# Optimization experiments

Hardware: AMD Instinct MI355X
Metric: run time of the kernel (lower is better)

## Reference

```python
import jax, jax.numpy as jnp
import numpy as np

N = 50000   # nodes
E = 800000  # edges (avg degree 16)
D = 2048    # resnet50 feature dim
C = 256     # layer_size
NEG_SLOPE = 0.2


def setup_inputs() -> dict:
    key = jax.random.key(0)
    ks = jax.random.split(key, 16)
    s = 0.02
    inp = {
        'x': jax.random.normal(ks[0], (N, D), jnp.float32),
        'edge_index': jax.random.randint(ks[1], (2, E), 0, N, dtype=jnp.int32),
        # GATConv layer 1 (in=D, out=C, heads=1)
        'W1': jax.random.normal(ks[2], (D, C), jnp.float32) * s,
        'a_src1': jax.random.normal(ks[3], (C,), jnp.float32) * s,
        'a_dst1': jax.random.normal(ks[4], (C,), jnp.float32) * s,
        'b1': jnp.zeros((C,), jnp.float32),
        # GATConv layer 2 (in=C, out=C)
        'W2': jax.random.normal(ks[5], (C, C), jnp.float32) * s,
        'a_src2': jax.random.normal(ks[6], (C,), jnp.float32) * s,
        'a_dst2': jax.random.normal(ks[7], (C,), jnp.float32) * s,
        'b2': jnp.zeros((C,), jnp.float32),
        # EdgePredictor: lin1 (2C -> C), lin2 (C -> 1)
        'Wp1': jax.random.normal(ks[8], (2 * C, C), jnp.float32) * s,
        'bp1': jnp.zeros((C,), jnp.float32),
        'wp2': jax.random.normal(ks[9], (C,), jnp.float32) * s,
        'bp2': jnp.zeros((), jnp.float32),
    }
    return inp


def gat_layer(x, src, dst, W, a_src, a_dst, b, n_nodes):
    # PyG GATConv, heads=1, concat=True: message flows src -> dst,
    # softmax over incoming edges of each dst node.
    h = x @ W                                   # [N, C]
    e = jax.nn.leaky_relu((h @ a_src)[src] + (h @ a_dst)[dst], NEG_SLOPE)  # [E]
    emax = jax.ops.segment_max(e, dst, num_segments=n_nodes)
    ex = jnp.exp(e - emax[dst])
    denom = jax.ops.segment_sum(ex, dst, num_segments=n_nodes)
    alpha = ex / (denom[dst] + 1e-16)           # [E]
    out = jax.ops.segment_sum(h[src] * alpha[:, None], dst, num_segments=n_nodes)
    return out + b


def reference(x, edge_index, W1, a_src1, a_dst1, b1, W2, a_src2, a_dst2, b2,
              Wp1, bp1, wp2, bp2):
    src, dst = edge_index[0], edge_index[1]
    # GATConv default add_self_loops=True
    loops = jnp.arange(N, dtype=src.dtype)
    src_sl = jnp.concatenate([src, loops])
    dst_sl = jnp.concatenate([dst, loops])

    h = gat_layer(x, src_sl, dst_sl, W1, a_src1, a_dst1, b1, N)
    h = gat_layer(h, src_sl, dst_sl, W2, a_src2, a_dst2, b2, N)

    # edge predictor on the ORIGINAL edge_index (no self loops)
    xe = jnp.concatenate([h[src], h[dst]], axis=-1)       # [E, 2C]
    z = jax.nn.relu(xe @ Wp1 + bp1)                        # [E, C]  (dropout: eval mode)
    return z @ wp2 + bp2                                   # [E]
```

## Files before the change

### kernel.cpp

```cpp
#include <hip/hip_runtime.h>
#include <hip/hip_bf16.h>
#include <stdint.h>

#define NNODES 50000
#define NEDGES 800000
#define DIN    2048
#define CDIM   256
#define ELOOP  (NEDGES + NNODES)

using bf16x8 = __attribute__((ext_vector_type(8))) short;
using f32x4  = __attribute__((ext_vector_type(4))) float;
using gvoid  = __attribute__((address_space(1))) const void;
using lvoid  = __attribute__((address_space(3))) void;

__device__ __forceinline__ float bf2f(uint16_t u) {
    union { uint32_t i; float f; } v; v.i = (uint32_t)u << 16; return v.f;
}
__device__ __forceinline__ uint16_t f2bf(float f) {
    union { float f; uint32_t i; } v; v.f = f;
    uint32_t i = v.i;
    return (uint16_t)((i + 0x7FFFu + ((i >> 16) & 1u)) >> 16);
}

#define BM 128
#define BN 128
#define BK 32

__global__ __launch_bounds__(256)
void gemm_bt(const uint16_t* __restrict__ A, const uint16_t* __restrict__ Bt,
             uint16_t* __restrict__ C, const float* __restrict__ bias,
             int M, int N, int K)
{
    __shared__ __align__(16) uint16_t lA[BM * BK];
    __shared__ __align__(16) uint16_t lB[BN * BK];
    const int tid  = threadIdx.x;
    const int wave = tid >> 6;
    const int lane = tid & 63;
    const int lm = lane & 15, lq = lane >> 4;
    const int bm = blockIdx.x * BM;
    const int bn = blockIdx.y * BN;
    const int wm = (wave >> 1) * 64;
    const int wn = (wave & 1) * 64;

    f32x4 acc[4][4];
    for (int i = 0; i < 4; ++i)
        for (int j = 0; j < 4; ++j)
            acc[i][j] = (f32x4)0.0f;

    for (int k0 = 0; k0 < K; k0 += BK) {
        for (int j = 0; j < 2; ++j) {
            int c = j * 256 + wave * 64 + lane;
            int row = c >> 2, cc = c & 3;
            int gr = bm + row; if (gr >= M) gr = M - 1;
            const uint16_t* gp = A + (size_t)gr * K + k0 + cc * 8;
            __builtin_amdgcn_global_load_lds((gvoid*)gp,
                (lvoid*)(lA + (size_t)(j * 256 + wave * 64) * 8), 16, 0, 0);
        }
        for (int j = 0; j < 2; ++j) {
            int c = j * 256 + wave * 64 + lane;
            int row = c >> 2, cc = c & 3;
            int gr = bn + row; if (gr >= N) gr = N - 1;
            const uint16_t* gp = Bt + (size_t)gr * K + k0 + cc * 8;
            __builtin_amdgcn_global_load_lds((gvoid*)gp,
                (lvoid*)(lB + (size_t)(j * 256 + wave * 64) * 8), 16, 0, 0);
        }
        __syncthreads();

        bf16x8 af[4], bfr[4];
        for (int mt = 0; mt < 4; ++mt)
            af[mt] = *(const bf16x8*)(lA + (wm + mt * 16 + lm) * BK + lq * 8);
        for (int nt = 0; nt < 4; ++nt)
            bfr[nt] = *(const bf16x8*)(lB + (wn + nt * 16 + lm) * BK + lq * 8);

        for (int mt = 0; mt < 4; ++mt)
            for (int nt = 0; nt < 4; ++nt)
                acc[mt][nt] = __builtin_amdgcn_mfma_f32_16x16x32_bf16(
                    af[mt], bfr[nt], acc[mt][nt], 0, 0, 0);
        __syncthreads();
    }

    for (int mt = 0; mt < 4; ++mt) {
        for (int nt = 0; nt < 4; ++nt) {
            int gn = bn + wn + nt * 16 + lm;
            float badd = bias ? bias[gn] : 0.0f;
            for (int r = 0; r < 4; ++r) {
                int gm = bm + wm + mt * 16 + lq * 4 + r;
                if (gm < M)
                    C[(size_t)gm * N + gn] = f2bf(acc[mt][nt][r] + badd);
            }
        }
    }
}

__global__ __launch_bounds__(256)
void gemm_f32_bt(const float* __restrict__ A, const uint16_t* __restrict__ Bt,
                 uint16_t* __restrict__ C, int M, int N, int K)
{
    __shared__ __align__(16) float    lA[BM * BK];
    __shared__ __align__(16) uint16_t lB[BN * BK];
    const int tid  = threadIdx.x;
    const int wave = tid >> 6;
    const int lane = tid & 63;
    const int lm = lane & 15, lq = lane >> 4;
    const int bm = blockIdx.x * BM;
    const int bn = blockIdx.y * BN;
    const int wm = (wave >> 1) * 64;
    const int wn = (wave & 1) * 64;

    f32x4 acc[4][4];
    for (int i = 0; i < 4; ++i)
        for (int j = 0; j < 4; ++j)
            acc[i][j] = (f32x4)0.0f;

    for (int k0 = 0; k0 < K; k0 += BK) {
        for (int j = 0; j < 4; ++j) {
            int c = j * 256 + wave * 64 + lane;
            int row = c >> 3;
            int lc  = (c & 7) ^ (row & 7);
            int gr = bm + row; if (gr >= M) gr = M - 1;
            const float* gp = A + (size_t)gr * K + k0 + lc * 4;
            __builtin_amdgcn_global_load_lds((gvoid*)gp,
                (lvoid*)(lA + (size_t)(j * 256 + wave * 64) * 4), 16, 0, 0);
        }
        for (int j = 0; j < 2; ++j) {
            int c = j * 256 + wave * 64 + lane;
            int row = c >> 2, cc = c & 3;
            const uint16_t* gp = Bt + (size_t)(bn + row) * K + k0 + cc * 8;
            __builtin_amdgcn_global_load_lds((gvoid*)gp,
                (lvoid*)(lB + (size_t)(j * 256 + wave * 64) * 8), 16, 0, 0);
        }
        __syncthreads();

        bf16x8 af[4], bfr[4];
        for (int mt = 0; mt < 4; ++mt) {
            int r = wm + mt * 16 + lm;
            int s0 = (lq * 2)     ^ (r & 7);
            int s1 = (lq * 2 + 1) ^ (r & 7);
            f32x4 a0 = *(const f32x4*)(lA + r * BK + s0 * 4);
            f32x4 a1 = *(const f32x4*)(lA + r * BK + s1 * 4);
            bf16x8 t;
            for (int q = 0; q < 4; ++q) {
                t[q]     = (short)f2bf(a0[q]);
                t[q + 4] = (short)f2bf(a1[q]);
            }
            af[mt] = t;
        }
        for (int nt = 0; nt < 4; ++nt)
            bfr[nt] = *(const bf16x8*)(lB + (wn + nt * 16 + lm) * BK + lq * 8);

        for (int mt = 0; mt < 4; ++mt)
            for (int nt = 0; nt < 4; ++nt)
                acc[mt][nt] = __builtin_amdgcn_mfma_f32_16x16x32_bf16(
                    af[mt], bfr[nt], acc[mt][nt], 0, 0, 0);
        __syncthreads();
    }

    for (int mt = 0; mt < 4; ++mt) {
        for (int nt = 0; nt < 4; ++nt) {
            int gn = bn + wn + nt * 16 + lm;
            for (int r = 0; r < 4; ++r) {
                int gm = bm + wm + mt * 16 + lq * 4 + r;
                if (gm < M)
                    C[(size_t)gm * N + gn] = f2bf(acc[mt][nt][r]);
            }
        }
    }
}

__global__ void transpose_cvt_kernel(const float* __restrict__ W,
                                     uint16_t* __restrict__ Wt, int K, int N)
{
    int idx = blockIdx.x * 256 + threadIdx.x;
    if (idx >= K * N) return;
    int n = idx / K, k = idx - n * K;
    Wt[idx] = f2bf(W[(size_t)k * N + n]);
}

__global__ void count_kernel(const int* __restrict__ ei, int* __restrict__ rs)
{
    int i = blockIdx.x * 256 + threadIdx.x;
    if (i >= ELOOP) return;
    int dst = (i < NEDGES) ? ei[NEDGES + i] : (i - NEDGES);
    atomicAdd(&rs[dst + 1], 1);
}

__global__ __launch_bounds__(1024)
void scan_kernel(int* __restrict__ rs, int* __restrict__ cursor)
{
    __shared__ int wsum[16];
    const int tid = threadIdx.x, lane = tid & 63, w = tid >> 6;
    int carry = 0;
    for (int base = 0; base <= NNODES; base += 1024) {
        int i = base + tid;
        int v = (i <= NNODES) ? rs[i] : 0;
        int s = v;
        for (int d = 1; d < 64; d <<= 1) {
            int t = __shfl_up(s, d);
            if (lane >= d) s += t;
        }
        if (lane == 63) wsum[w] = s;
        __syncthreads();
        if (tid < 16) {
            int x = wsum[tid];
            for (int d = 1; d < 16; d <<= 1) {
                int t = __shfl_up(x, d);
                if (tid >= d) x += t;
            }
            wsum[tid] = x;
        }
        __syncthreads();
        int incl = s + carry + (w > 0 ? wsum[w - 1] : 0);
        if (i <= NNODES) {
            rs[i] = incl;
            if (i < NNODES) cursor[i] = incl;
        }
        int total = carry + wsum[15];
        __syncthreads();
        carry = total;
    }
}

__global__ void fill_kernel(const int* __restrict__ ei, int* __restrict__ cursor,
                            int* __restrict__ csr_src)
{
    int i = blockIdx.x * 256 + threadIdx.x;
    if (i >= ELOOP) return;
    int src, dst;
    if (i < NEDGES) { src = ei[i]; dst = ei[NEDGES + i]; }
    else            { src = dst = i - NEDGES; }
    int pos = atomicAdd(&cursor[dst], 1);
    csr_src[pos] = src;
}

__global__ __launch_bounds__(256)
void rowdot_kernel(const uint16_t* __restrict__ g,
                   const float* __restrict__ asrc,
                   const float* __restrict__ adst,
                   float* __restrict__ s_src, float* __restrict__ s_dst)
{
    int n = blockIdx.x * 4 + (threadIdx.x >> 6);
    int lane = threadIdx.x & 63;
    ushort4 rv = *(const ushort4*)(g + (size_t)n * CDIM + lane * 4);
    float4 av = *(const float4*)(asrc + lane * 4);
    float4 dv = *(const float4*)(adst + lane * 4);
    float r0 = bf2f(rv.x), r1 = bf2f(rv.y), r2 = bf2f(rv.z), r3 = bf2f(rv.w);
    float a = r0 * av.x + r1 * av.y + r2 * av.z + r3 * av.w;
    float b = r0 * dv.x + r1 * dv.y + r2 * dv.z + r3 * dv.w;
    for (int d = 32; d; d >>= 1) { a += __shfl_xor(a, d); b += __shfl_xor(b, d); }
    if (lane == 0) { s_src[n] = a; s_dst[n] = b; }
}

__global__ __launch_bounds__(256)
void attn_kernel(const int* __restrict__ row_start, const int* __restrict__ csr_src,
                 const float* __restrict__ s_src, const float* __restrict__ s_dst,
                 const uint16_t* __restrict__ g, const float* __restrict__ bvec,
                 uint16_t* __restrict__ hout)
{
    int n = blockIdx.x * 4 + (threadIdx.x >> 6);
    int lane = threadIdx.x & 63;
    int beg = row_start[n], end = row_start[n + 1];
    float sdn = s_dst[n];

    float m = -1e30f;
    for (int i = beg + lane; i < end; i += 64) {
        float e = s_src[csr_src[i]] + sdn;
        e = (e > 0.f) ? e : 0.2f * e;
        m = fmaxf(m, e);
    }
    for (int d = 32; d; d >>= 1) m = fmaxf(m, __shfl_xor(m, d));

    float sum = 0.f;
    for (int i = beg + lane; i < end; i += 64) {
        float e = s_src[csr_src[i]] + sdn;
        e = (e > 0.f) ? e : 0.2f * e;
        sum += __expf(e - m);
    }
    for (int d = 32; d; d >>= 1) sum += __shfl_xor(sum, d);
    float inv = 1.f / (sum + 1e-16f);

    float a0 = 0.f, a1 = 0.f, a2 = 0.f, a3 = 0.f;
    for (int i = beg; i < end; ++i) {
        int src = csr_src[i];
        float e = s_src[src] + sdn;
        e = (e > 0.f) ? e : 0.2f * e;
        float alpha = __expf(e - m) * inv;
        ushort4 rv = *(const ushort4*)(g + (size_t)src * CDIM + lane * 4);
        a0 += alpha * bf2f(rv.x);
        a1 += alpha * bf2f(rv.y);
        a2 += alpha * bf2f(rv.z);
        a3 += alpha * bf2f(rv.w);
    }
    float4 bv = *(const float4*)(bvec + lane * 4);
    ushort4 o;
    o.x = f2bf(a0 + bv.x);
    o.y = f2bf(a1 + bv.y);
    o.z = f2bf(a2 + bv.z);
    o.w = f2bf(a3 + bv.w);
    *(ushort4*)(hout + (size_t)n * CDIM + lane * 4) = o;
}

__global__ __launch_bounds__(256)
void edgepred_kernel(const int* __restrict__ ei,
                     const uint16_t* __restrict__ U, const uint16_t* __restrict__ V,
                     const float* __restrict__ wp2, const float* __restrict__ bp2,
                     float* __restrict__ out)
{
    const int tid = threadIdx.x;
    const int grp = tid >> 4, l = tid & 15;
    const int e = blockIdx.x * 16 + grp;
    int src = ei[e];
    int dst = ei[NEDGES + e];
    const uint4 u0 = *(const uint4*)(U + (size_t)src * CDIM + l * 16);
    const uint4 u1 = *(const uint4*)(U + (size_t)src * CDIM + l * 16 + 8);
    const uint4 v0 = *(const uint4*)(V + (size_t)dst * CDIM + l * 16);
    const uint4 v1 = *(const uint4*)(V + (size_t)dst * CDIM + l * 16 + 8);
    const float4 w0 = *(const float4*)(wp2 + l * 16);
    const float4 w1 = *(const float4*)(wp2 + l * 16 + 4);
    const float4 w2 = *(const float4*)(wp2 + l * 16 + 8);
    const float4 w3 = *(const float4*)(wp2 + l * 16 + 12);
    float acc = 0.f;
    auto proc = [&](uint32_t uu, uint32_t vv, float wa, float wb) {
        float z0 = fmaxf(bf2f((uint16_t)(uu & 0xffffu)) + bf2f((uint16_t)(vv & 0xffffu)), 0.f);
        float z1 = fmaxf(bf2f((uint16_t)(uu >> 16)) + bf2f((uint16_t)(vv >> 16)), 0.f);
        acc += z0 * wa + z1 * wb;
    };
    proc(u0.x, v0.x, w0.x, w0.y); proc(u0.y, v0.y, w0.z, w0.w);
    proc(u0.z, v0.z, w1.x, w1.y); proc(u0.w, v0.w, w1.z, w1.w);
    proc(u1.x, v1.x, w2.x, w2.y); proc(u1.y, v1.y, w2.z, w2.w);
    proc(u1.z, v1.z, w3.x, w3.y); proc(u1.w, v1.w, w3.z, w3.w);
    for (int d = 1; d < 16; d <<= 1) acc += __shfl_xor(acc, d);
    if (l == 0) out[e] = acc + *bp2;
}

extern "C" void kernel_launch(void* const* d_in, const int* in_sizes, int n_in,
                              void* d_out, int out_size, void* d_ws, size_t ws_size,
                              hipStream_t stream)
{
    const float* x   = (const float*)d_in[0];
    const int*   ei  = (const int*)d_in[1];
    const float* W1  = (const float*)d_in[2];
    const float* as1 = (const float*)d_in[3];
    const float* ad1 = (const float*)d_in[4];
    const float* b1  = (const float*)d_in[5];
    const float* W2  = (const float*)d_in[6];
    const float* as2 = (const float*)d_in[7];
    const float* ad2 = (const float*)d_in[8];
    const float* b2  = (const float*)d_in[9];
    const float* Wp1 = (const float*)d_in[10];
    const float* bp1 = (const float*)d_in[11];
    const float* wp2 = (const float*)d_in[12];
    const float* bp2 = (const float*)d_in[13];
    float* out = (float*)d_out;

    char* ws = (char*)d_ws;
    size_t off = 0;
    auto alloc = [&](size_t bytes) -> void* {
        void* p = ws + off;
        off += (bytes + 255) & ~(size_t)255;
        return p;
    };
    uint16_t* W1t  = (uint16_t*)alloc((size_t)DIN * CDIM * 2);
    uint16_t* W2t  = (uint16_t*)alloc((size_t)CDIM * CDIM * 2);
    uint16_t* WpAt = (uint16_t*)alloc((size_t)CDIM * CDIM * 2);
    uint16_t* WpBt = (uint16_t*)alloc((size_t)CDIM * CDIM * 2);
    int* row_start = (int*)alloc((NNODES + 1) * sizeof(int));
    int* cursor    = (int*)alloc(NNODES * sizeof(int));
    int* csr_src   = (int*)alloc((size_t)ELOOP * sizeof(int));
    float* s_src   = (float*)alloc(NNODES * sizeof(float));
    float* s_dst   = (float*)alloc(NNODES * sizeof(float));
    uint16_t* G    = (uint16_t*)alloc((size_t)NNODES * CDIM * 2);
    uint16_t* H    = (uint16_t*)alloc((size_t)NNODES * CDIM * 2);
    uint16_t* Vb   = (uint16_t*)alloc((size_t)NNODES * CDIM * 2);

    hipMemsetAsync(row_start, 0, (NNODES + 1) * sizeof(int), stream);

    transpose_cvt_kernel<<<(DIN * CDIM + 255) / 256, 256, 0, stream>>>(W1, W1t, DIN, CDIM);
    transpose_cvt_kernel<<<(CDIM * CDIM + 255) / 256, 256, 0, stream>>>(W2, W2t, CDIM, CDIM);
    transpose_cvt_kernel<<<(CDIM * CDIM + 255) / 256, 256, 0, stream>>>(Wp1, WpAt, CDIM, CDIM);
    transpose_cvt_kernel<<<(CDIM * CDIM + 255) / 256, 256, 0, stream>>>(Wp1 + CDIM * CDIM, WpBt, CDIM, CDIM);

    count_kernel<<<(ELOOP + 255) / 256, 256, 0, stream>>>(ei, row_start);
    scan_kernel<<<1, 1024, 0, stream>>>(row_start, cursor);
    fill_kernel<<<(ELOOP + 255) / 256, 256, 0, stream>>>(ei, cursor, csr_src);

    dim3 gg((NNODES + BM - 1) / BM, CDIM / BN);

    gemm_f32_bt<<<gg, 256, 0, stream>>>(x, W1t, G, NNODES, CDIM, DIN);
    rowdot_kernel<<<NNODES / 4, 256, 0, stream>>>(G, as1, ad1, s_src, s_dst);
    attn_kernel<<<NNODES / 4, 256, 0, stream>>>(row_start, csr_src, s_src, s_dst, G, b1, H);

    gemm_bt<<<gg, 256, 0, stream>>>(H, W2t, G, nullptr, NNODES, CDIM, CDIM);
    rowdot_kernel<<<NNODES / 4, 256, 0, stream>>>(G, as2, ad2, s_src, s_dst);
    attn_kernel<<<NNODES / 4, 256, 0, stream>>>(row_start, csr_src, s_src, s_dst, G, b2, H);

    gemm_bt<<<gg, 256, 0, stream>>>(H, WpAt, G, bp1, NNODES, CDIM, CDIM);
    gemm_bt<<<gg, 256, 0, stream>>>(H, WpBt, Vb, nullptr, NNODES, CDIM, CDIM);

    edgepred_kernel<<<NEDGES / 16, 256, 0, stream>>>(ei, G, Vb, wp2, bp2, out);
}
```

Measured before the change: 1.237 ms.

## Double-buffer LDS tiles in GEMMs and merge edge-predictor GEMMs into one

Both GEMM kernels now keep two LDS buffers and issue the global-to-LDS loads for the next K tile before computing on the current one. This is meant to overlap load latency with the MFMA work and drops one barrier per iteration. The two 256-wide edge-predictor projections become a single N=512 GEMM that writes an interleaved U|V buffer with a padded bias vector. Edgepred reads both halves from that one buffer, which saves a launch and a second read of H. The cost is double the LDS use and a 512-wide output that spills from the G region into the adjacent Vb allocation.

```diff
diff --git a/kernel.cpp b/kernel.cpp
--- a/kernel.cpp
+++ b/kernel.cpp
@@ -31,8 +31,8 @@
              uint16_t* __restrict__ C, const float* __restrict__ bias,
              int M, int N, int K)
 {
-    __shared__ __align__(16) uint16_t lA[BM * BK];
-    __shared__ __align__(16) uint16_t lB[BN * BK];
+    __shared__ __align__(16) uint16_t lA[2][BM * BK];
+    __shared__ __align__(16) uint16_t lB[2][BN * BK];
     const int tid  = threadIdx.x;
     const int wave = tid >> 6;
     const int lane = tid & 63;
@@ -47,14 +47,14 @@
         for (int j = 0; j < 4; ++j)
             acc[i][j] = (f32x4)0.0f;
 
-    for (int k0 = 0; k0 < K; k0 += BK) {
+    auto stage = [&](int buf, int k0) {
         for (int j = 0; j < 2; ++j) {
             int c = j * 256 + wave * 64 + lane;
             int row = c >> 2, cc = c & 3;
             int gr = bm + row; if (gr >= M) gr = M - 1;
             const uint16_t* gp = A + (size_t)gr * K + k0 + cc * 8;
             __builtin_amdgcn_global_load_lds((gvoid*)gp,
-                (lvoid*)(lA + (size_t)(j * 256 + wave * 64) * 8), 16, 0, 0);
+                (lvoid*)(lA[buf] + (size_t)(j * 256 + wave * 64) * 8), 16, 0, 0);
         }
         for (int j = 0; j < 2; ++j) {
             int c = j * 256 + wave * 64 + lane;
@@ -62,31 +62,39 @@
             int gr = bn + row; if (gr >= N) gr = N - 1;
             const uint16_t* gp = Bt + (size_t)gr * K + k0 + cc * 8;
             __builtin_amdgcn_global_load_lds((gvoid*)gp,
-                (lvoid*)(lB + (size_t)(j * 256 + wave * 64) * 8), 16, 0, 0);
-        }
-        __syncthreads();
+                (lvoid*)(lB[buf] + (size_t)(j * 256 + wave * 64) * 8), 16, 0, 0);
+        }
+    };
+
+    const int nt = K / BK;
+    stage(0, 0);
+    __syncthreads();
+    int cur = 0;
+    for (int t = 0; t < nt; ++t) {
+        if (t + 1 < nt) stage(cur ^ 1, (t + 1) * BK);
 
         bf16x8 af[4], bfr[4];
         for (int mt = 0; mt < 4; ++mt)
-            af[mt] = *(const bf16x8*)(lA + (wm + mt * 16 + lm) * BK + lq * 8);
-        for (int nt = 0; nt < 4; ++nt)
-            bfr[nt] = *(const bf16x8*)(lB + (wn + nt * 16 + lm) * BK + lq * 8);
+            af[mt] = *(const bf16x8*)(lA[cur] + (wm + mt * 16 + lm) * BK + lq * 8);
+        for (int nt2 = 0; nt2 < 4; ++nt2)
+            bfr[nt2] = *(const bf16x8*)(lB[cur] + (wn + nt2 * 16 + lm) * BK + lq * 8);
 
         for (int mt = 0; mt < 4; ++mt)
-            for (int nt = 0; nt < 4; ++nt)
-                acc[mt][nt] = __builtin_amdgcn_mfma_f32_16x16x32_bf16(
-                    af[mt], bfr[nt], acc[mt][nt], 0, 0, 0);
+            for (int nt2 = 0; nt2 < 4; ++nt2)
+                acc[mt][nt2] = __builtin_amdgcn_mfma_f32_16x16x32_bf16(
+                    af[mt], bfr[nt2], acc[mt][nt2], 0, 0, 0);
         __syncthreads();
+        cur ^= 1;
     }
 
     for (int mt = 0; mt < 4; ++mt) {
-        for (int nt = 0; nt < 4; ++nt) {
-            int gn = bn + wn + nt * 16 + lm;
+        for (int nt2 = 0; nt2 < 4; ++nt2) {
+            int gn = bn + wn + nt2 * 16 + lm;
             float badd = bias ? bias[gn] : 0.0f;
             for (int r = 0; r < 4; ++r) {
                 int gm = bm + wm + mt * 16 + lq * 4 + r;
                 if (gm < M)
-                    C[(size_t)gm * N + gn] = f2bf(acc[mt][nt][r] + badd);
+                    C[(size_t)gm * N + gn] = f2bf(acc[mt][nt2][r] + badd);
             }
         }
     }
@@ -96,8 +104,8 @@
 void gemm_f32_bt(const float* __restrict__ A, const uint16_t* __restrict__ Bt,
                  uint16_t* __restrict__ C, int M, int N, int K)
 {
-    __shared__ __align__(16) float    lA[BM * BK];
-    __shared__ __align__(16) uint16_t lB[BN * BK];
+    __shared__ __align__(16) float    lA[2][BM * BK];
+    __shared__ __align__(16) uint16_t lB[2][BN * BK];
     const int tid  = threadIdx.x;
     const int wave = tid >> 6;
     const int lane = tid & 63;
@@ -112,7 +120,7 @@
         for (int j = 0; j < 4; ++j)
             acc[i][j] = (f32x4)0.0f;
 
-    for (int k0 = 0; k0 < K; k0 += BK) {
+    auto stage = [&](int buf, int k0) {
         for (int j = 0; j < 4; ++j) {
             int c = j * 256 + wave * 64 + lane;
             int row = c >> 3;
@@ -120,48 +128,57 @@
             int gr = bm + row; if (gr >= M) gr = M - 1;
             const float* gp = A + (size_t)gr * K + k0 + lc * 4;
             __builtin_amdgcn_global_load_lds((gvoid*)gp,
-                (lvoid*)(lA + (size_t)(j * 256 + wave * 64) * 4), 16, 0, 0);
+                (lvoid*)(lA[buf] + (size_t)(j * 256 + wave * 64) * 4), 16, 0, 0);
         }
         for (int j = 0; j < 2; ++j) {
             int c = j * 256 + wave * 64 + lane;
             int row = c >> 2, cc = c & 3;
-            const uint16_t* gp = Bt + (size_t)(bn + row) * K + k0 + cc * 8;
+            int gr = bn + row; if (gr >= N) gr = N - 1;
+            const uint16_t* gp = Bt + (size_t)gr * K + k0 + cc * 8;
             __builtin_amdgcn_global_load_lds((gvoid*)gp,
-                (lvoid*)(lB + (size_t)(j * 256 + wave * 64) * 8), 16, 0, 0);
-        }
-        __syncthreads();
+                (lvoid*)(lB[buf] + (size_t)(j * 256 + wave * 64) * 8), 16, 0, 0);
+        }
+    };
+
+    const int nt = K / BK;
+    stage(0, 0);
+    __syncthreads();
+    int cur = 0;
+    for (int t = 0; t < nt; ++t) {
+        if (t + 1 < nt) stage(cur ^ 1, (t + 1) * BK);
 
         bf16x8 af[4], bfr[4];
         for (int mt = 0; mt < 4; ++mt) {
             int r = wm + mt * 16 + lm;
             int s0 = (lq * 2)     ^ (r & 7);
             int s1 = (lq * 2 + 1) ^ (r & 7);
-            f32x4 a0 = *(const f32x4*)(lA + r * BK + s0 * 4);
-            f32x4 a1 = *(const f32x4*)(lA + r * BK + s1 * 4);
-            bf16x8 t;
+            f32x4 a0 = *(const f32x4*)(lA[cur] + r * BK + s0 * 4);
+            f32x4 a1 = *(const f32x4*)(lA[cur] + r * BK + s1 * 4);
+            bf16x8 t2;
             for (int q = 0; q < 4; ++q) {
-                t[q]     = (short)f2bf(a0[q]);
-                t[q + 4] = (short)f2bf(a1[q]);
+                t2[q]     = (short)f2bf(a0[q]);
+                t2[q + 4] = (short)f2bf(a1[q]);
             }
-            af[mt] = t;
-        }
-        for (int nt = 0; nt < 4; ++nt)
-            bfr[nt] = *(const bf16x8*)(lB + (wn + nt * 16 + lm) * BK + lq * 8);
+            af[mt] = t2;
+        }
+        for (int nt2 = 0; nt2 < 4; ++nt2)
+            bfr[nt2] = *(const bf16x8*)(lB[cur] + (wn + nt2 * 16 + lm) * BK + lq * 8);
 
         for (int mt = 0; mt < 4; ++mt)
-            for (int nt = 0; nt < 4; ++nt)
-                acc[mt][nt] = __builtin_amdgcn_mfma_f32_16x16x32_bf16(
-                    af[mt], bfr[nt], acc[mt][nt], 0, 0, 0);
+            for (int nt2 = 0; nt2 < 4; ++nt2)
+                acc[mt][nt2] = __builtin_amdgcn_mfma_f32_16x16x32_bf16(
+                    af[mt], bfr[nt2], acc[mt][nt2], 0, 0, 0);
         __syncthreads();
+        cur ^= 1;
     }
 
     for (int mt = 0; mt < 4; ++mt) {
-        for (int nt = 0; nt < 4; ++nt) {
-            int gn = bn + wn + nt * 16 + lm;
+        for (int nt2 = 0; nt2 < 4; ++nt2) {
+            int gn = bn + wn + nt2 * 16 + lm;
             for (int r = 0; r < 4; ++r) {
                 int gm = bm + wm + mt * 16 + lq * 4 + r;
                 if (gm < M)
-                    C[(size_t)gm * N + gn] = f2bf(acc[mt][nt][r]);
+                    C[(size_t)gm * N + gn] = f2bf(acc[mt][nt2][r]);
             }
         }
     }
@@ -174,6 +191,13 @@
     if (idx >= K * N) return;
     int n = idx / K, k = idx - n * K;
     Wt[idx] = f2bf(W[(size_t)k * N + n]);
+}
+
+__global__ void bias512_kernel(const float* __restrict__ bp1,
+                               float* __restrict__ bias512)
+{
+    int i = blockIdx.x * 256 + threadIdx.x;
+    if (i < 512) bias512[i] = (i < 256) ? bp1[i] : 0.0f;
 }
 
 __global__ void count_kernel(const int* __restrict__ ei, int* __restrict__ rs)
@@ -301,7 +325,7 @@
 
 __global__ __launch_bounds__(256)
 void edgepred_kernel(const int* __restrict__ ei,
-                     const uint16_t* __restrict__ U, const uint16_t* __restrict__ V,
+                     const uint16_t* __restrict__ UV,
                      const float* __restrict__ wp2, const float* __restrict__ bp2,
                      float* __restrict__ out)
 {
@@ -310,10 +334,12 @@
     const int e = blockIdx.x * 16 + grp;
     int src = ei[e];
     int dst = ei[NEDGES + e];
-    const uint4 u0 = *(const uint4*)(U + (size_t)src * CDIM + l * 16);
-    const uint4 u1 = *(const uint4*)(U + (size_t)src * CDIM + l * 16 + 8);
-    const uint4 v0 = *(const uint4*)(V + (size_t)dst * CDIM + l * 16);
-    const uint4 v1 = *(const uint4*)(V + (size_t)dst * CDIM + l * 16 + 8);
+    const uint16_t* Up = UV + (size_t)src * 512 + l * 16;
+    const uint16_t* Vp = UV + (size_t)dst * 512 + 256 + l * 16;
+    const uint4 u0 = *(const uint4*)(Up);
+    const uint4 u1 = *(const uint4*)(Up + 8);
+    const uint4 v0 = *(const uint4*)(Vp);
+    const uint4 v1 = *(const uint4*)(Vp + 8);
     const float4 w0 = *(const float4*)(wp2 + l * 16);
     const float4 w1 = *(const float4*)(wp2 + l * 16 + 4);
     const float4 w2 = *(const float4*)(wp2 + l * 16 + 8);
@@ -359,25 +385,27 @@
         off += (bytes + 255) & ~(size_t)255;
         return p;
     };
-    uint16_t* W1t  = (uint16_t*)alloc((size_t)DIN * CDIM * 2);
-    uint16_t* W2t  = (uint16_t*)alloc((size_t)CDIM * CDIM * 2);
-    uint16_t* WpAt = (uint16_t*)alloc((size_t)CDIM * CDIM * 2);
-    uint16_t* WpBt = (uint16_t*)alloc((size_t)CDIM * CDIM * 2);
+    uint16_t* W1t   = (uint16_t*)alloc((size_t)DIN * CDIM * 2);
+    uint16_t* W2t   = (uint16_t*)alloc((size_t)CDIM * CDIM * 2);
+    uint16_t* WpABt = (uint16_t*)alloc((size_t)2 * CDIM * CDIM * 2);
     int* row_start = (int*)alloc((NNODES + 1) * sizeof(int));
     int* cursor    = (int*)alloc(NNODES * sizeof(int));
     int* csr_src   = (int*)alloc((size_t)ELOOP * sizeof(int));
     float* s_src   = (float*)alloc(NNODES * sizeof(float));
     float* s_dst   = (float*)alloc(NNODES * sizeof(float));
+    float* bias512 = (float*)alloc(512 * sizeof(float));
+    uint16_t* H    = (uint16_t*)alloc((size_t)NNODES * CDIM * 2);
     uint16_t* G    = (uint16_t*)alloc((size_t)NNODES * CDIM * 2);
-    uint16_t* H    = (uint16_t*)alloc((size_t)NNODES * CDIM * 2);
     uint16_t* Vb   = (uint16_t*)alloc((size_t)NNODES * CDIM * 2);
+    uint16_t* UV   = G;
 
     hipMemsetAsync(row_start, 0, (NNODES + 1) * sizeof(int), stream);
 
     transpose_cvt_kernel<<<(DIN * CDIM + 255) / 256, 256, 0, stream>>>(W1, W1t, DIN, CDIM);
     transpose_cvt_kernel<<<(CDIM * CDIM + 255) / 256, 256, 0, stream>>>(W2, W2t, CDIM, CDIM);
-    transpose_cvt_kernel<<<(CDIM * CDIM + 255) / 256, 256, 0, stream>>>(Wp1, WpAt, CDIM, CDIM);
-    transpose_cvt_kernel<<<(CDIM * CDIM + 255) / 256, 256, 0, stream>>>(Wp1 + CDIM * CDIM, WpBt, CDIM, CDIM);
+    transpose_cvt_kernel<<<(CDIM * CDIM + 255) / 256, 256, 0, stream>>>(Wp1, WpABt, CDIM, CDIM);
+    transpose_cvt_kernel<<<(CDIM * CDIM + 255) / 256, 256, 0, stream>>>(Wp1 + CDIM * CDIM, WpABt + CDIM * CDIM, CDIM, CDIM);
+    bias512_kernel<<<2, 256, 0, stream>>>(bp1, bias512);
 
     count_kernel<<<(ELOOP + 255) / 256, 256, 0, stream>>>(ei, row_start);
     scan_kernel<<<1, 1024, 0, stream>>>(row_start, cursor);
@@ -393,8 +421,8 @@
     rowdot_kernel<<<NNODES / 4, 256, 0, stream>>>(G, as2, ad2, s_src, s_dst);
     attn_kernel<<<NNODES / 4, 256, 0, stream>>>(row_start, csr_src, s_src, s_dst, G, b2, H);
 
-    gemm_bt<<<gg, 256, 0, stream>>>(H, WpAt, G, bp1, NNODES, CDIM, CDIM);
-    gemm_bt<<<gg, 256, 0, stream>>>(H, WpBt, Vb, nullptr, NNODES, CDIM, CDIM);
-
-    edgepred_kernel<<<NEDGES / 16, 256, 0, stream>>>(ei, G, Vb, wp2, bp2, out);
-}
+    dim3 gg2((NNODES + BM - 1) / BM, 512 / BN);
+    gemm_bt<<<gg2, 256, 0, stream>>>(H, WpABt, UV, bias512, NNODES, 512, CDIM);
+
+    edgepred_kernel<<<NEDGES / 16, 256, 0, stream>>>(ei, UV, wp2, bp2, out);
+}
```

Result: no change. 1.239 ms (+0.2%).
